# Optimization experiments

Hardware: AMD Instinct MI355X
Metric: run time of the kernel (lower is better)

The kernel has to match this reference:

```python
import jax, jax.numpy as jnp
import numpy as np
import math

B, S, D, H = 4, 2048, 1024, 16
HD = D // H  # 64

def setup_inputs() -> dict:
    key = jax.random.key(0)
    ks = jax.random.split(key, 4)
    x = jax.random.normal(ks[0], (B, S, D), dtype=jnp.float32)
    # causal mask, True = attend (precomputed as in the original usage)
    mask = jnp.tril(jnp.ones((S, S), dtype=bool))[None, None, :, :]
    c_attn_w = jax.random.normal(ks[1], (D, 3 * D), dtype=jnp.float32) * 0.02
    c_attn_b = jnp.zeros((3 * D,), dtype=jnp.float32)
    c_proj_w = jax.random.normal(ks[2], (D, D), dtype=jnp.float32) * 0.02
    c_proj_b = jnp.zeros((D,), dtype=jnp.float32)
    return {"x": x, "mask": mask, "c_attn_w": c_attn_w, "c_attn_b": c_attn_b,
            "c_proj_w": c_proj_w, "c_proj_b": c_proj_b}

def reference(x, mask, c_attn_w, c_attn_b, c_proj_w, c_proj_b):
    b, s, d = x.shape
    # c_attn: Conv1D acts as Linear with transposed weight convention
    qkv = x @ c_attn_w + c_attn_b                      # [B,S,3D]
    q, k, v = jnp.split(qkv, 3, axis=-1)
    q = q.reshape(b, s, H, HD).transpose(0, 2, 1, 3)   # [B,H,S,hd]
    k = k.reshape(b, s, H, HD).transpose(0, 2, 1, 3)   # [B,H,S,hd]
    v = v.reshape(b, s, H, HD).transpose(0, 2, 1, 3)   # [B,H,S,hd]
    # scores, scale by sqrt(head_dim) (done unconditionally in _attn)
    w = jnp.einsum('bhqd,bhkd->bhqk', q, k) / math.sqrt(HD)
    # masked_fill_(1 - mask, -10000.0)
    w = jnp.where(mask, w, jnp.float32(-10000.0))
    w = jax.nn.softmax(w, axis=-1)                     # attn_dropout p=0
    a = jnp.einsum('bhqk,bhkd->bhqd', w, v)            # [B,H,S,hd]
    a = a.transpose(0, 2, 1, 3).reshape(b, s, d)       # merge heads
    out = a @ c_proj_w + c_proj_b                      # resid_dropout p=0
    return out
```

## Files before the change

kernel.cpp:

```cpp
#include <hip/hip_runtime.h>

#define SEQ  2048
#define DIM  1024
#define NH   16
#define HD   64
#define NB   4

typedef __bf16 bf16_t;
typedef bf16_t bf16x8 __attribute__((ext_vector_type(8)));
typedef float  floatx4 __attribute__((ext_vector_type(4)));

#define MFMA16(a, b, c) __builtin_amdgcn_mfma_f32_16x16x32_bf16((a), (b), (c), 0, 0, 0)

__device__ __forceinline__ void gl_lds16(const bf16_t* g, bf16_t* l) {
    __builtin_amdgcn_global_load_lds(
        (const __attribute__((address_space(1))) void*)g,
        (__attribute__((address_space(3))) void*)l,
        16, 0, 0);
}

__global__ __launch_bounds__(256) void cvt_f32_bf16(
    const float* __restrict__ in, bf16_t* __restrict__ out, int n) {
    const int i = (blockIdx.x * 256 + threadIdx.x) * 4;
    const float4 v = *(const float4*)(in + i);
    out[i + 0] = (bf16_t)v.x;
    out[i + 1] = (bf16_t)v.y;
    out[i + 2] = (bf16_t)v.z;
    out[i + 3] = (bf16_t)v.w;
}

__global__ __launch_bounds__(256) void transpose_f32_bf16(
    const float* __restrict__ in, bf16_t* __restrict__ out, int R, int C) {
    __shared__ bf16_t t[32][33];
    const int c0 = blockIdx.x * 32, r0 = blockIdx.y * 32;
    const int tx = threadIdx.x & 31, ty = threadIdx.x >> 5;
#pragma unroll
    for (int i = 0; i < 32; i += 8)
        t[ty + i][tx] = (bf16_t)in[(r0 + ty + i) * C + c0 + tx];
    __syncthreads();
#pragma unroll
    for (int i = 0; i < 32; i += 8)
        out[(c0 + ty + i) * R + r0 + tx] = t[tx][ty + i];
}

template <int MODE>
__global__ __launch_bounds__(256, 2) void gemm128(
    const bf16_t* __restrict__ A, const bf16_t* __restrict__ Bt,
    const float* __restrict__ bias, int K,
    bf16_t* __restrict__ Qo, bf16_t* __restrict__ Ko, bf16_t* __restrict__ Vo,
    float* __restrict__ Co) {
    __shared__ __align__(16) bf16_t smem[MODE == 0 ? 128 * 136 : 128 * 64];
    bf16_t* Al = smem;
    bf16_t* Bl = smem + 128 * 32;

    const int tid = threadIdx.x;
    const int m0 = blockIdx.y * 128, n0 = blockIdx.x * 128;
    const int w = tid >> 6, lane = tid & 63;
    const int l15 = lane & 15, quad = lane >> 4;
    const int wm = (w & 1) * 64, wn = (w >> 1) * 64;

    floatx4 acc[4][4] = {};

    const bf16_t* aptr = A + (m0 + (tid >> 2)) * K + (tid & 3) * 8;
    const bf16_t* bptr = Bt + (n0 + (tid >> 2)) * K + (tid & 3) * 8;
    bf16_t* al = Al + tid * 8;
    bf16_t* bl = Bl + tid * 8;

    for (int k0 = 0; k0 < K; k0 += 32) {
        gl_lds16(aptr, al);
        gl_lds16(aptr + 64 * K, al + 2048);
        gl_lds16(bptr, bl);
        gl_lds16(bptr + 64 * K, bl + 2048);
        aptr += 32;
        bptr += 32;
        __syncthreads();

        bf16x8 af[4], bfr[4];
#pragma unroll
        for (int i = 0; i < 4; i++)
            af[i] = *(const bf16x8*)&Al[(wm + i * 16 + l15) * 32 + quad * 8];
#pragma unroll
        for (int j = 0; j < 4; j++)
            bfr[j] = *(const bf16x8*)&Bl[(wn + j * 16 + l15) * 32 + quad * 8];
#pragma unroll
        for (int i = 0; i < 4; i++)
#pragma unroll
            for (int j = 0; j < 4; j++)
                acc[i][j] = MFMA16(af[i], bfr[j], acc[i][j]);
        __syncthreads();
    }

    if (MODE == 0) {
        bf16_t* Cl = smem;
        const int which = n0 >> 10;
        const float qs = (which == 0) ? 0.125f : 1.0f;
#pragma unroll
        for (int j = 0; j < 4; j++) {
            const int ncol = wn + j * 16 + l15;
            const float bv = bias[n0 + ncol];
#pragma unroll
            for (int i = 0; i < 4; i++)
#pragma unroll
                for (int r = 0; r < 4; r++) {
                    const int mrow = wm + i * 16 + quad * 4 + r;
                    Cl[mrow * 136 + ncol] = (bf16_t)((acc[i][j][r] + bv) * qs);
                }
        }
        __syncthreads();

        if (which < 2) {
            const int row = tid >> 1, ch = (tid & 1) << 6;
            const int m = m0 + row, b = m >> 11, s = m & 2047;
            const int h = ((n0 & 1023) >> 6) + (ch >> 6);
            bf16_t* dst = (which == 0 ? Qo : Ko) + ((size_t)(b * NH + h) * SEQ + s) * HD;
            const bf16_t* src = Cl + row * 136 + ch;
#pragma unroll
            for (int g = 0; g < 8; g++)
                *(bf16x8*)(dst + g * 8) = *(const bf16x8*)(src + g * 8);
        } else {
            const int dl = tid & 127, sh = (tid >> 7) << 6;
            const int h = ((n0 & 1023) >> 6) + (dl >> 6), d = dl & 63;
            const int b = m0 >> 11, sbase = (m0 & 2047) + sh;
            bf16_t* dst = Vo + ((size_t)(b * NH + h) * HD + d) * SEQ + sbase;
#pragma unroll
            for (int g = 0; g < 8; g++) {
                bf16x8 tv;
#pragma unroll
                for (int e = 0; e < 8; e++)
                    tv[e] = Cl[(sh + g * 8 + e) * 136 + dl];
                *(bf16x8*)(dst + g * 8) = tv;
            }
        }
    } else {
#pragma unroll
        for (int j = 0; j < 4; j++) {
            const int n = n0 + wn + j * 16 + l15;
            const float bv = bias[n];
#pragma unroll
            for (int i = 0; i < 4; i++)
#pragma unroll
                for (int r = 0; r < 4; r++) {
                    const int m = m0 + wm + i * 16 + quad * 4 + r;
                    Co[m * 1024 + n] = acc[i][j][r] + bv;
                }
        }
    }
}

__global__ __launch_bounds__(256, 2) void attn2q(
    const bf16_t* __restrict__ Q, const bf16_t* __restrict__ Kg,
    const bf16_t* __restrict__ Vt, bf16_t* __restrict__ Aout) {
    __shared__ bf16_t Ks[64 * 64];
    __shared__ bf16_t Vs[64 * 64];
    __shared__ bf16_t Ps[128 * 64];

    const int bh = blockIdx.y;
    const int px = (blockIdx.x + (bh >> 3)) & 7;
    const int qtA = 15 - px, qtB = px;
    const int nkA = 2 * qtA + 2, nkB = 2 * qtB + 2;

    const int tid = threadIdx.x, w = tid >> 6, lane = tid & 63;
    const int l15 = lane & 15, quad = lane >> 4;
    const int b = bh >> 4, hd = bh & 15;
    const int xk = l15 & 7;

    bf16x8 aqA[2][2], aqB[2][2];
#pragma unroll
    for (int i = 0; i < 2; i++) {
        const bf16_t* qrA = Q + (size_t)(bh * SEQ + qtA * 128 + w * 32 + i * 16 + l15) * HD;
        const bf16_t* qrB = Q + (size_t)(bh * SEQ + qtB * 128 + w * 32 + i * 16 + l15) * HD;
#pragma unroll
        for (int h = 0; h < 2; h++) {
            aqA[i][h] = *(const bf16x8*)(qrA + h * 32 + quad * 8);
            aqB[i][h] = *(const bf16x8*)(qrB + h * 32 + quad * 8);
        }
    }

    floatx4 oA[2][4] = {}, oB[2][4] = {};
    float liA[2][4] = {}, liB[2][4] = {};

    const int r_st = tid >> 2, g0 = tid & 3;
    const bf16_t* kgl = Kg + (size_t)bh * SEQ * HD + (size_t)r_st * HD;
    const bf16_t* vgl = Vt + (size_t)bh * HD * SEQ + (size_t)r_st * SEQ;
    const int sw0 = ((g0 ^ (r_st & 7)) * 8);
    const int sw1 = (((g0 + 4) ^ (r_st & 7)) * 8);
    bf16_t* ksw = Ks + r_st * 64;
    bf16_t* vsw = Vs + r_st * 64;

    auto proc = [&](int qt, bf16x8 (&aq)[2][2], floatx4 (&o)[2][4],
                    float (&li)[2][4], int kt) {
        const int qrow0 = qt * 128 + w * 32;
        bf16x8 bk[4][2];
#pragma unroll
        for (int j = 0; j < 4; j++) {
            const int n = j * 16 + l15;
#pragma unroll
            for (int h = 0; h < 2; h++)
                bk[j][h] = *(const bf16x8*)&Ks[n * 64 + (((h * 4 + quad) ^ xk) * 8)];
        }
        floatx4 z[2][4] = {};
#pragma unroll
        for (int i = 0; i < 2; i++)
#pragma unroll
            for (int j = 0; j < 4; j++) {
                z[i][j] = MFMA16(aq[i][0], bk[j][0], z[i][j]);
                z[i][j] = MFMA16(aq[i][1], bk[j][1], z[i][j]);
            }
        const bool full = (kt * 64 + 63) <= qrow0;
#pragma unroll
        for (int i = 0; i < 2; i++)
#pragma unroll
            for (int j = 0; j < 4; j++) {
                const int kg = kt * 64 + j * 16 + l15;
#pragma unroll
                for (int r = 0; r < 4; r++) {
                    float e = __expf(z[i][j][r]);
                    const int prow = w * 32 + i * 16 + quad * 4 + r;
                    if (!full && kg > prow + qt * 128) e = 0.f;
                    li[i][r] += e;
                    const int col = j * 16 + l15;
                    Ps[prow * 64 + ((((col >> 3) ^ (prow & 7)) << 3) | (col & 7))] =
                        (bf16_t)e;
                }
            }
        __builtin_amdgcn_s_waitcnt(0xC07F);
        bf16x8 ap[2][2];
#pragma unroll
        for (int i = 0; i < 2; i++) {
            const int row = w * 32 + i * 16 + l15;
#pragma unroll
            for (int kk = 0; kk < 2; kk++)
                ap[i][kk] = *(const bf16x8*)&Ps[row * 64 +
                                               (((kk * 4 + quad) ^ (row & 7)) << 3)];
        }
        bf16x8 bv[4][2];
#pragma unroll
        for (int j = 0; j < 4; j++) {
            const int n = j * 16 + l15;
#pragma unroll
            for (int kk = 0; kk < 2; kk++)
                bv[j][kk] = *(const bf16x8*)&Vs[n * 64 + (((kk * 4 + quad) ^ xk) * 8)];
        }
#pragma unroll
        for (int i = 0; i < 2; i++)
#pragma unroll
            for (int j = 0; j < 4; j++) {
                o[i][j] = MFMA16(ap[i][0], bv[j][0], o[i][j]);
                o[i][j] = MFMA16(ap[i][1], bv[j][1], o[i][j]);
            }
    };

    for (int kt = 0; kt < nkA; ++kt) {
        const bf16x8 k0 = *(const bf16x8*)(kgl + kt * 64 * HD + g0 * 8);
        const bf16x8 k1 = *(const bf16x8*)(kgl + kt * 64 * HD + (g0 + 4) * 8);
        const bf16x8 v0 = *(const bf16x8*)(vgl + kt * 64 + g0 * 8);
        const bf16x8 v1 = *(const bf16x8*)(vgl + kt * 64 + (g0 + 4) * 8);
        *(bf16x8*)(ksw + sw0) = k0;
        *(bf16x8*)(ksw + sw1) = k1;
        *(bf16x8*)(vsw + sw0) = v0;
        *(bf16x8*)(vsw + sw1) = v1;
        __syncthreads();

        proc(qtA, aqA, oA, liA, kt);
        if (kt < nkB) proc(qtB, aqB, oB, liB, kt);
        __syncthreads();
    }

#pragma unroll
    for (int t = 0; t < 2; t++) {
        const int qt = t == 0 ? qtA : qtB;
        floatx4(&o)[2][4] = t == 0 ? oA : oB;
        float(&li)[2][4] = t == 0 ? liA : liB;
#pragma unroll
        for (int i = 0; i < 2; i++)
#pragma unroll
            for (int r = 0; r < 4; r++) {
                float s = li[i][r];
#pragma unroll
                for (int off = 1; off < 16; off <<= 1)
                    s += __shfl_xor(s, off, 64);
                const float inv = 1.0f / s;
                const int srow = qt * 128 + w * 32 + i * 16 + quad * 4 + r;
                bf16_t* orow = Aout + (size_t)(b * SEQ + srow) * DIM + hd * HD;
#pragma unroll
                for (int j = 0; j < 4; j++)
                    orow[j * 16 + l15] = (bf16_t)(o[i][j][r] * inv);
            }
    }
}

extern "C" void kernel_launch(void* const* d_in, const int* in_sizes, int n_in,
                              void* d_out, int out_size, void* d_ws, size_t ws_size,
                              hipStream_t stream) {
    const float* x        = (const float*)d_in[0];
    const float* c_attn_w = (const float*)d_in[2];
    const float* c_attn_b = (const float*)d_in[3];
    const float* c_proj_w = (const float*)d_in[4];
    const float* c_proj_b = (const float*)d_in[5];
    float* out = (float*)d_out;

    char* ws = (char*)d_ws;
    bf16_t* xb     = (bf16_t*)ws; ws += (size_t)NB * SEQ * DIM * 2;
    bf16_t* wqkvT  = (bf16_t*)ws; ws += (size_t)3072 * 1024 * 2;
    bf16_t* wprojT = (bf16_t*)ws; ws += (size_t)1024 * 1024 * 2;
    bf16_t* Qb  = (bf16_t*)ws; ws += (size_t)NB * NH * SEQ * HD * 2;
    bf16_t* Kb  = (bf16_t*)ws; ws += (size_t)NB * NH * SEQ * HD * 2;
    bf16_t* Vtb = (bf16_t*)ws; ws += (size_t)NB * NH * SEQ * HD * 2;
    bf16_t* Ab  = (bf16_t*)ws; ws += (size_t)NB * SEQ * DIM * 2;

    const int nx = NB * SEQ * DIM;
    cvt_f32_bf16<<<nx / 1024, 256, 0, stream>>>(x, xb, nx);
    transpose_f32_bf16<<<dim3(96, 32), 256, 0, stream>>>(c_attn_w, wqkvT, 1024, 3072);
    transpose_f32_bf16<<<dim3(32, 32), 256, 0, stream>>>(c_proj_w, wprojT, 1024, 1024);

    gemm128<0><<<dim3(24, 64), 256, 0, stream>>>(xb, wqkvT, c_attn_b, 1024,
                                                 Qb, Kb, Vtb, nullptr);

    attn2q<<<dim3(8, NB * NH), 256, 0, stream>>>(Qb, Kb, Vtb, Ab);

    gemm128<1><<<dim3(8, 64), 256, 0, stream>>>(Ab, wprojT, c_proj_b, 1024,
                                                nullptr, nullptr, nullptr, out);
}
```

Before: 295.2 us.

## Fuse prep kernels, pair KV tiles per barrier, transpose QK MFMA for packed P stores

Merges the x conversion and the two weight transposes into one prep launch, removing two kernel launches. The attention kernel now stages two K/V tiles per sync, halving barriers at the cost of doubled K/V LDS. It also swaps the MFMA operands for QK^T so each lane holds four consecutive key columns of one query row. That allows packed 4-element P stores to LDS, a single running row sum per lane, and a cheaper final reduction. The larger LDS footprint may hurt occupancy, and the pair loop assumes nkA is even, which holds for nkA = 2*qtA + 2.

Result: faster. 278.7 us (-5.6%).

```diff
diff --git a/kernel.cpp b/kernel.cpp
--- a/kernel.cpp
+++ b/kernel.cpp
@@ -8,6 +8,7 @@
 
 typedef __bf16 bf16_t;
 typedef bf16_t bf16x8 __attribute__((ext_vector_type(8)));
+typedef bf16_t bf16x4 __attribute__((ext_vector_type(4)));
 typedef float  floatx4 __attribute__((ext_vector_type(4)));
 
 #define MFMA16(a, b, c) __builtin_amdgcn_mfma_f32_16x16x32_bf16((a), (b), (c), 0, 0, 0)
@@ -19,21 +20,35 @@
         16, 0, 0);
 }
 
-__global__ __launch_bounds__(256) void cvt_f32_bf16(
-    const float* __restrict__ in, bf16_t* __restrict__ out, int n) {
-    const int i = (blockIdx.x * 256 + threadIdx.x) * 4;
-    const float4 v = *(const float4*)(in + i);
-    out[i + 0] = (bf16_t)v.x;
-    out[i + 1] = (bf16_t)v.y;
-    out[i + 2] = (bf16_t)v.z;
-    out[i + 3] = (bf16_t)v.w;
-}
-
-__global__ __launch_bounds__(256) void transpose_f32_bf16(
-    const float* __restrict__ in, bf16_t* __restrict__ out, int R, int C) {
+__global__ __launch_bounds__(256) void prep(
+    const float* __restrict__ x, bf16_t* __restrict__ xb,
+    const float* __restrict__ wqkv, bf16_t* __restrict__ wqkvT,
+    const float* __restrict__ wproj, bf16_t* __restrict__ wprojT) {
+    const int bid = blockIdx.x, tid = threadIdx.x;
+    if (bid < 8192) {
+        const int i = (bid * 256 + tid) * 4;
+        const float4 v = *(const float4*)(x + i);
+        xb[i + 0] = (bf16_t)v.x;
+        xb[i + 1] = (bf16_t)v.y;
+        xb[i + 2] = (bf16_t)v.z;
+        xb[i + 3] = (bf16_t)v.w;
+        return;
+    }
     __shared__ bf16_t t[32][33];
-    const int c0 = blockIdx.x * 32, r0 = blockIdx.y * 32;
-    const int tx = threadIdx.x & 31, ty = threadIdx.x >> 5;
+    const float* in;
+    bf16_t* out;
+    int R, C, bx, by;
+    if (bid < 8192 + 3072) {
+        const int idx = bid - 8192;
+        in = wqkv; out = wqkvT; R = 1024; C = 3072;
+        bx = idx % 96; by = idx / 96;
+    } else {
+        const int idx = bid - 11264;
+        in = wproj; out = wprojT; R = 1024; C = 1024;
+        bx = idx & 31; by = idx >> 5;
+    }
+    const int c0 = bx * 32, r0 = by * 32;
+    const int tx = tid & 31, ty = tid >> 5;
 #pragma unroll
     for (int i = 0; i < 32; i += 8)
         t[ty + i][tx] = (bf16_t)in[(r0 + ty + i) * C + c0 + tx];
@@ -150,8 +165,8 @@
 __global__ __launch_bounds__(256, 2) void attn2q(
     const bf16_t* __restrict__ Q, const bf16_t* __restrict__ Kg,
     const bf16_t* __restrict__ Vt, bf16_t* __restrict__ Aout) {
-    __shared__ bf16_t Ks[64 * 64];
-    __shared__ bf16_t Vs[64 * 64];
+    __shared__ bf16_t Ks[2 * 64 * 64];
+    __shared__ bf16_t Vs[2 * 64 * 64];
     __shared__ bf16_t Ps[128 * 64];
 
     const int bh = blockIdx.y;
@@ -177,52 +192,57 @@
     }
 
     floatx4 oA[2][4] = {}, oB[2][4] = {};
-    float liA[2][4] = {}, liB[2][4] = {};
+    float liA[2] = {}, liB[2] = {};
 
     const int r_st = tid >> 2, g0 = tid & 3;
     const bf16_t* kgl = Kg + (size_t)bh * SEQ * HD + (size_t)r_st * HD;
     const bf16_t* vgl = Vt + (size_t)bh * HD * SEQ + (size_t)r_st * SEQ;
     const int sw0 = ((g0 ^ (r_st & 7)) * 8);
     const int sw1 = (((g0 + 4) ^ (r_st & 7)) * 8);
-    bf16_t* ksw = Ks + r_st * 64;
-    bf16_t* vsw = Vs + r_st * 64;
 
     auto proc = [&](int qt, bf16x8 (&aq)[2][2], floatx4 (&o)[2][4],
-                    float (&li)[2][4], int kt) {
-        const int qrow0 = qt * 128 + w * 32;
+                    float (&li)[2], int kt, int sub) {
+        const bf16_t* Ksub = Ks + sub * 4096;
+        const bf16_t* Vsub = Vs + sub * 4096;
         bf16x8 bk[4][2];
 #pragma unroll
         for (int j = 0; j < 4; j++) {
             const int n = j * 16 + l15;
 #pragma unroll
             for (int h = 0; h < 2; h++)
-                bk[j][h] = *(const bf16x8*)&Ks[n * 64 + (((h * 4 + quad) ^ xk) * 8)];
+                bk[j][h] = *(const bf16x8*)&Ksub[n * 64 + (((h * 4 + quad) ^ xk) * 8)];
         }
         floatx4 z[2][4] = {};
 #pragma unroll
         for (int i = 0; i < 2; i++)
 #pragma unroll
             for (int j = 0; j < 4; j++) {
-                z[i][j] = MFMA16(aq[i][0], bk[j][0], z[i][j]);
-                z[i][j] = MFMA16(aq[i][1], bk[j][1], z[i][j]);
-            }
-        const bool full = (kt * 64 + 63) <= qrow0;
-#pragma unroll
-        for (int i = 0; i < 2; i++)
+                z[i][j] = MFMA16(bk[j][0], aq[i][0], z[i][j]);
+                z[i][j] = MFMA16(bk[j][1], aq[i][1], z[i][j]);
+            }
+#pragma unroll
+        for (int i = 0; i < 2; i++) {
+            const int qbase = qt * 128 + w * 32 + i * 16;
+            const int qrow_l = qbase + l15;
+            const bool full = (kt * 64 + 63) <= qbase;
+            const int prow = w * 32 + i * 16 + l15;
+            bf16_t* pbase = Ps + prow * 64;
+            const int rx = prow & 7;
 #pragma unroll
             for (int j = 0; j < 4; j++) {
-                const int kg = kt * 64 + j * 16 + l15;
+                const int kg0 = kt * 64 + j * 16 + quad * 4;
+                bf16x4 pk;
 #pragma unroll
                 for (int r = 0; r < 4; r++) {
                     float e = __expf(z[i][j][r]);
-                    const int prow = w * 32 + i * 16 + quad * 4 + r;
-                    if (!full && kg > prow + qt * 128) e = 0.f;
-                    li[i][r] += e;
-                    const int col = j * 16 + l15;
-                    Ps[prow * 64 + ((((col >> 3) ^ (prow & 7)) << 3) | (col & 7))] =
-                        (bf16_t)e;
+                    if (!full && kg0 + r > qrow_l) e = 0.f;
+                    li[i] += e;
+                    pk[r] = (bf16_t)e;
                 }
-            }
+                const int g = 2 * j + (quad >> 1);
+                *(bf16x4*)(pbase + (((g ^ rx) << 3) | ((quad & 1) << 2))) = pk;
+            }
+        }
         __builtin_amdgcn_s_waitcnt(0xC07F);
         bf16x8 ap[2][2];
 #pragma unroll
@@ -239,7 +259,7 @@
             const int n = j * 16 + l15;
 #pragma unroll
             for (int kk = 0; kk < 2; kk++)
-                bv[j][kk] = *(const bf16x8*)&Vs[n * 64 + (((kk * 4 + quad) ^ xk) * 8)];
+                bv[j][kk] = *(const bf16x8*)&Vsub[n * 64 + (((kk * 4 + quad) ^ xk) * 8)];
         }
 #pragma unroll
         for (int i = 0; i < 2; i++)
@@ -250,19 +270,28 @@
             }
     };
 
-    for (int kt = 0; kt < nkA; ++kt) {
-        const bf16x8 k0 = *(const bf16x8*)(kgl + kt * 64 * HD + g0 * 8);
-        const bf16x8 k1 = *(const bf16x8*)(kgl + kt * 64 * HD + (g0 + 4) * 8);
-        const bf16x8 v0 = *(const bf16x8*)(vgl + kt * 64 + g0 * 8);
-        const bf16x8 v1 = *(const bf16x8*)(vgl + kt * 64 + (g0 + 4) * 8);
-        *(bf16x8*)(ksw + sw0) = k0;
-        *(bf16x8*)(ksw + sw1) = k1;
-        *(bf16x8*)(vsw + sw0) = v0;
-        *(bf16x8*)(vsw + sw1) = v1;
-        __syncthreads();
-
-        proc(qtA, aqA, oA, liA, kt);
-        if (kt < nkB) proc(qtB, aqB, oB, liB, kt);
+    for (int ktp = 0; ktp < nkA; ktp += 2) {
+#pragma unroll
+        for (int sub = 0; sub < 2; ++sub) {
+            const int kt = ktp + sub;
+            const bf16x8 k0 = *(const bf16x8*)(kgl + kt * 64 * HD + g0 * 8);
+            const bf16x8 k1 = *(const bf16x8*)(kgl + kt * 64 * HD + (g0 + 4) * 8);
+            const bf16x8 v0 = *(const bf16x8*)(vgl + kt * 64 + g0 * 8);
+            const bf16x8 v1 = *(const bf16x8*)(vgl + kt * 64 + (g0 + 4) * 8);
+            bf16_t* ks = Ks + sub * 4096 + r_st * 64;
+            bf16_t* vs = Vs + sub * 4096 + r_st * 64;
+            *(bf16x8*)(ks + sw0) = k0;
+            *(bf16x8*)(ks + sw1) = k1;
+            *(bf16x8*)(vs + sw0) = v0;
+            *(bf16x8*)(vs + sw1) = v1;
+        }
+        __syncthreads();
+#pragma unroll
+        for (int sub = 0; sub < 2; ++sub) {
+            const int kt = ktp + sub;
+            proc(qtA, aqA, oA, liA, kt, sub);
+            if (kt < nkB) proc(qtB, aqB, oB, liB, kt, sub);
+        }
         __syncthreads();
     }
 
@@ -270,22 +299,23 @@
     for (int t = 0; t < 2; t++) {
         const int qt = t == 0 ? qtA : qtB;
         floatx4(&o)[2][4] = t == 0 ? oA : oB;
-        float(&li)[2][4] = t == 0 ? liA : liB;
-#pragma unroll
-        for (int i = 0; i < 2; i++)
+        float(&li)[2] = t == 0 ? liA : liB;
+#pragma unroll
+        for (int i = 0; i < 2; i++) {
+            float s = li[i];
+            s += __shfl_xor(s, 16, 64);
+            s += __shfl_xor(s, 32, 64);
 #pragma unroll
             for (int r = 0; r < 4; r++) {
-                float s = li[i][r];
-#pragma unroll
-                for (int off = 1; off < 16; off <<= 1)
-                    s += __shfl_xor(s, off, 64);
-                const float inv = 1.0f / s;
+                const float sv = __shfl(s, quad * 4 + r, 64);
+                const float inv = 1.0f / sv;
                 const int srow = qt * 128 + w * 32 + i * 16 + quad * 4 + r;
                 bf16_t* orow = Aout + (size_t)(b * SEQ + srow) * DIM + hd * HD;
 #pragma unroll
                 for (int j = 0; j < 4; j++)
                     orow[j * 16 + l15] = (bf16_t)(o[i][j][r] * inv);
             }
+        }
     }
 }
 
@@ -308,10 +338,7 @@
     bf16_t* Vtb = (bf16_t*)ws; ws += (size_t)NB * NH * SEQ * HD * 2;
     bf16_t* Ab  = (bf16_t*)ws; ws += (size_t)NB * SEQ * DIM * 2;
 
-    const int nx = NB * SEQ * DIM;
-    cvt_f32_bf16<<<nx / 1024, 256, 0, stream>>>(x, xb, nx);
-    transpose_f32_bf16<<<dim3(96, 32), 256, 0, stream>>>(c_attn_w, wqkvT, 1024, 3072);
-    transpose_f32_bf16<<<dim3(32, 32), 256, 0, stream>>>(c_proj_w, wprojT, 1024, 1024);
+    prep<<<12288, 256, 0, stream>>>(x, xb, c_attn_w, wqkvT, c_proj_w, wprojT);
 
     gemm128<0><<<dim3(24, 64), 256, 0, stream>>>(xb, wqkvT, c_attn_b, 1024,
                                                  Qb, Kb, Vtb, nullptr);
```
